# Performance work log

Measured on AMD Instinct MI355X. Metric: run time of the kernel, lower is better.

Reference implementation:

```python
import jax, jax.numpy as jnp
import numpy as np
from jax import lax

N_FRAMES = 256

def _conv(x, w, b):
    # NCHW conv, stride 3 on mel axis (matches MOSNet CNN that collapses mels 81->27->9->3->1)
    y = lax.conv_general_dilated(x, w, window_strides=(1, 3),
                                 padding=((1, 1), (1, 1)),
                                 dimension_numbers=('NCHW', 'OIHW', 'NCHW'))
    return jax.nn.relu(y + b[None, :, None, None])

def _lstm(x, Wih, Whh, bih, bhh, reverse=False):
    # x: [T, B, D] -> hs: [T, B, H]; PyTorch gate order i, f, g, o
    Bsz, H = x.shape[1], Whh.shape[1]
    bias = bih + bhh
    def step(carry, xt):
        h, c = carry
        z = xt @ Wih.T + h @ Whh.T + bias
        i, f, g, o = jnp.split(z, 4, axis=-1)
        c = jax.nn.sigmoid(f) * c + jax.nn.sigmoid(i) * jnp.tanh(g)
        h = jax.nn.sigmoid(o) * jnp.tanh(c)
        return (h, c), h
    init = (jnp.zeros((Bsz, H), x.dtype), jnp.zeros((Bsz, H), x.dtype))
    _, hs = lax.scan(step, init, x, reverse=reverse)
    return hs

def setup_inputs():
    key = jax.random.key(0)
    ks = jax.random.split(key, 24)
    B, T, M = 16, 4096, 81
    chans = [1, 16, 32, 64, 128]
    H = 128
    FC_IN = 2 * H * N_FRAMES  # 65536
    FC_H = 128
    s = 0.05
    inp = {'audio': jax.random.normal(ks[0], (B, T, M), jnp.float32),
           'sample_lengths': jnp.full((B,), T, dtype=jnp.int32)}
    for li in range(4):
        inp['w%d' % li] = jax.random.normal(ks[1 + 2 * li], (chans[li + 1], chans[li], 3, 3), jnp.float32) * s
        inp['b%d' % li] = jnp.zeros((chans[li + 1],), jnp.float32)
    D = chans[-1]
    for d, off in (('f', 9), ('b', 13)):
        inp['Wih_' + d] = jax.random.normal(ks[off], (4 * H, D), jnp.float32) * s
        inp['Whh_' + d] = jax.random.normal(ks[off + 1], (4 * H, H), jnp.float32) * s
        inp['bih_' + d] = jnp.zeros((4 * H,), jnp.float32)
        inp['bhh_' + d] = jnp.zeros((4 * H,), jnp.float32)
    inp['fc1_w'] = jax.random.normal(ks[17], (FC_H, FC_IN), jnp.float32) * 0.005
    inp['fc1_b'] = jnp.zeros((FC_H,), jnp.float32)
    inp['fs_w'] = jax.random.normal(ks[18], (1, FC_H), jnp.float32) * s
    inp['fs_b'] = jnp.zeros((1,), jnp.float32)
    return inp

def reference(audio, w0, b0, w1, b1, w2, b2, w3, b3,
              Wih_f, Whh_f, bih_f, bhh_f, Wih_b, Whh_b, bih_b, bhh_b,
              fc1_w, fc1_b, fs_w, fs_b, sample_lengths):
    B, T, M = audio.shape
    F = T // N_FRAMES  # all lengths == T, multiple of N_FRAMES -> all frames full
    x = audio.reshape(B * F, 1, N_FRAMES, M)   # [BF, 1, nf, mels]
    for w, b in ((w0, b0), (w1, b1), (w2, b2), (w3, b3)):
        x = _conv(x, w, b)                      # mel axis 81->27->9->3->1
    x = x[..., 0].transpose(2, 0, 1)            # [nf, BF, C]
    h_f = _lstm(x, Wih_f, Whh_f, bih_f, bhh_f)
    h_b = _lstm(x, Wih_b, Whh_b, bih_b, bhh_b, reverse=True)
    h = jnp.concatenate([h_f, h_b], axis=-1).transpose(1, 0, 2)  # [BF, nf, 2H]
    flat = h.reshape(B * F, -1)                 # time-major flatten, matches view(1,-1)
    z = jax.nn.relu(flat @ fc1_w.T + fc1_b)     # dropout is identity at inference
    score = jax.nn.sigmoid(z @ fs_w.T + fs_b) * 4.0 + 1.0  # mos range [1,5]
    frames = score.reshape(B, F)
    utt = frames.mean(axis=1)
    return utt, frames
```

## Files before the change

### kernel.cpp

```cpp
#include <hip/hip_runtime.h>
#include <hip/hip_fp16.h>

#define BF 256
#define TSTEPS 256

typedef _Float16 h8_t __attribute__((ext_vector_type(8)));
typedef _Float16 h4_t __attribute__((ext_vector_type(4)));
typedef float f4_t __attribute__((ext_vector_type(4)));

union H8 { uint4 u; h8_t v; };
union H4 { uint2 u; h4_t v; };

static __device__ __forceinline__ float sigmoidf_(float x) {
    return 1.f / (1.f + __expf(-x));
}
static __device__ __forceinline__ float tanhf_(float x) {
    return 1.f - 2.f / (__expf(2.f * x) + 1.f);
}

static __device__ __forceinline__ void pack_one(const float* __restrict__ src,
                                                __half* __restrict__ dst,
                                                int OC, int IC, int KS,
                                                int oc_str, int ic_str, int k_str, int i) {
    int grp = KS / 4;
    int j = i % grp;
    int oc = (i / grp) % OC;
    int g = (i / (grp * OC)) & 3;
    int chunk = i / (grp * OC * 4);
    int CPK = IC / KS;
    int cc = chunk % CPK;
    int khw = chunk / CPK;
    int ic = cc * KS + g * grp + j;
    dst[i] = __float2half(src[(long)oc * oc_str + (long)ic * ic_str + khw * k_str]);
}

__global__ __launch_bounds__(256) void prep_k(
        const float* __restrict__ w0, const float* __restrict__ w1,
        const float* __restrict__ w2, const float* __restrict__ w3,
        const float* __restrict__ Wihf, const float* __restrict__ Wihb,
        const float* __restrict__ Whhf, const float* __restrict__ Whhb,
        float* __restrict__ w0t, __half* __restrict__ w1p,
        __half* __restrict__ w2p, __half* __restrict__ w3p,
        __half* __restrict__ wfp, __half* __restrict__ wbp,
        __half* __restrict__ whhfp, __half* __restrict__ whhbp) {
    int i = blockIdx.x * 256 + threadIdx.x;
    if (i < 144) { int oc = i / 9, rem = i % 9; w0t[rem * 16 + oc] = w0[i]; return; }
    i -= 144;
    if (i < 4608) { pack_one(w1, w1p, 32, 16, 16, 144, 9, 1, i); return; }
    i -= 4608;
    if (i < 18432) { pack_one(w2, w2p, 64, 32, 32, 288, 9, 1, i); return; }
    i -= 18432;
    if (i < 73728) { pack_one(w3, w3p, 128, 64, 32, 576, 9, 1, i); return; }
    i -= 73728;
    if (i < 65536) { pack_one(Wihf, wfp, 512, 128, 32, 128, 1, 0, i); return; }
    i -= 65536;
    if (i < 65536) { pack_one(Wihb, wbp, 512, 128, 32, 128, 1, 0, i); return; }
    i -= 65536;
    if (i < 65536) { pack_one(Whhf, whhfp, 512, 128, 32, 128, 1, 0, i); return; }
    i -= 65536;
    if (i < 65536) { pack_one(Whhb, whhbp, 512, 128, 32, 128, 1, 0, i); return; }
}

__global__ void pack_wf16(const float* __restrict__ src, __half* __restrict__ dst,
                          int OC, int IC, int KS,
                          int oc_str, int ic_str, int k_str, int total) {
    int i = blockIdx.x * 256 + threadIdx.x;
    if (i >= total) return;
    pack_one(src, dst, OC, IC, KS, oc_str, ic_str, k_str, i);
}

__global__ __launch_bounds__(256) void conv0_k(const float* __restrict__ in,
                                               const float* __restrict__ wT,
                                               const float* __restrict__ bias,
                                               __half* __restrict__ out) {
    __shared__ float wsm[9][16];
    __shared__ float bs[16];
    int tid = threadIdx.x;
    if (tid < 144) wsm[tid / 16][tid % 16] = wT[tid];
    if (tid < 16) bs[tid] = bias[tid];
    __syncthreads();
    int gid = blockIdx.x * 256 + tid;
    int ow = gid % 27;
    int t = (gid / 27) % 256;
    int bf = gid / (27 * 256);
    float acc[16];
#pragma unroll
    for (int o = 0; o < 16; o++) acc[o] = bs[o];
    int iw0 = ow * 3 - 1;
#pragma unroll
    for (int kh = 0; kh < 3; kh++) {
        int tt = t + kh - 1;
        if ((unsigned)tt >= 256u) continue;
        const float* ip = in + ((long)bf * 256 + tt) * 81;
#pragma unroll
        for (int kw = 0; kw < 3; kw++) {
            int iw = iw0 + kw;
            if ((unsigned)iw >= 81u) continue;
            float x = ip[iw];
#pragma unroll
            for (int o = 0; o < 16; o++) acc[o] += x * wsm[kh * 3 + kw][o];
        }
    }
    __half2* op = (__half2*)(out + (long)gid * 16);
#pragma unroll
    for (int o = 0; o < 8; o++)
        op[o] = __floats2half2_rn(fmaxf(acc[2 * o], 0.f), fmaxf(acc[2 * o + 1], 0.f));
}

template<int IC, int OC, int WIN, int WOUT, int KS>
__global__ __launch_bounds__(256) void convM_k(const __half* __restrict__ in,
                                               const __half* __restrict__ wp,
                                               const float* __restrict__ bias,
                                               __half* __restrict__ out) {
    constexpr int NT = OC / 16;
    constexpr int CPK = IC / KS;
    constexpr int NCHUNK = 9 * CPK;
    constexpr int GRP = KS / 4;
    int tid = threadIdx.x;
    int lane = tid & 63;
    int wv = tid >> 6;
    int l15 = lane & 15;
    int g = lane >> 4;
    int m = blockIdx.x * 64 + wv * 16 + l15;
    int ow = m % WOUT;
    int t = (m / WOUT) % 256;
    int bf = m / (WOUT * 256);

    f4_t acc[NT];
#pragma unroll
    for (int nt = 0; nt < NT; nt++)
#pragma unroll
        for (int r = 0; r < 4; r++) acc[nt][r] = 0.f;

#pragma unroll
    for (int chunk = 0; chunk < NCHUNK; chunk++) {
        int khw = chunk / CPK, cc = chunk % CPK;
        int kh = khw / 3;
        int kw = khw - kh * 3;
        int tt = t + kh - 1;
        int iw = ow * 3 + kw - 1;
        bool ok = ((unsigned)tt < 256u) && ((unsigned)iw < (unsigned)WIN);
        long aoff = ok ? (((long)(bf * 256 + tt) * WIN + iw) * IC + cc * KS + g * GRP) : 0;
        if constexpr (KS == 32) {
            H8 af;
            af.u = *(const uint4*)(in + aoff);
            if (!ok) af.u = make_uint4(0u, 0u, 0u, 0u);
#pragma unroll
            for (int nt = 0; nt < NT; nt++) {
                H8 bf8;
                bf8.u = *(const uint4*)(wp + ((long)(chunk * 4 + g) * OC + nt * 16 + l15) * GRP);
                acc[nt] = __builtin_amdgcn_mfma_f32_16x16x32_f16(af.v, bf8.v, acc[nt], 0, 0, 0);
            }
        } else {
            H4 af;
            af.u = *(const uint2*)(in + aoff);
            if (!ok) af.u = make_uint2(0u, 0u);
#pragma unroll
            for (int nt = 0; nt < NT; nt++) {
                H4 bf4;
                bf4.u = *(const uint2*)(wp + ((long)(chunk * 4 + g) * OC + nt * 16 + l15) * GRP);
                acc[nt] = __builtin_amdgcn_mfma_f32_16x16x16f16(af.v, bf4.v, acc[nt], 0, 0, 0);
            }
        }
    }
    int orow = blockIdx.x * 64 + wv * 16 + g * 4;
#pragma unroll
    for (int nt = 0; nt < NT; nt++) {
        int oc = nt * 16 + l15;
        float b = bias[oc];
#pragma unroll
        for (int r = 0; r < 4; r++) {
            float v = fmaxf(acc[nt][r] + b, 0.f);
            out[(long)(orow + r) * OC + oc] = __float2half(v);
        }
    }
}

__global__ __launch_bounds__(256) void gates_k(const __half* __restrict__ X,
                                               const __half* __restrict__ wpf,
                                               const __half* __restrict__ wpb,
                                               const float* __restrict__ bf1,
                                               const float* __restrict__ bf2,
                                               const float* __restrict__ bb1,
                                               const float* __restrict__ bb2,
                                               __half* __restrict__ Gf,
                                               __half* __restrict__ Gb) {
    int dir = blockIdx.z;
    const __half* wp = dir ? wpb : wpf;
    const float* b1 = dir ? bb1 : bf1;
    const float* b2 = dir ? bb2 : bf2;
    __half* G = dir ? Gb : Gf;
    int tid = threadIdx.x;
    int lane = tid & 63;
    int wv = tid >> 6;
    int l15 = lane & 15;
    int g = lane >> 4;
    long r0 = (long)blockIdx.x * 128 + wv * 32;
    int n0 = blockIdx.y * 128;

    f4_t acc[2][8];
#pragma unroll
    for (int s = 0; s < 2; s++)
#pragma unroll
        for (int nt = 0; nt < 8; nt++)
#pragma unroll
            for (int r = 0; r < 4; r++) acc[s][nt][r] = 0.f;

#pragma unroll
    for (int chunk = 0; chunk < 4; chunk++) {
        H8 a0, a1;
        a0.u = *(const uint4*)(X + (r0 + l15) * 128 + chunk * 32 + g * 8);
        a1.u = *(const uint4*)(X + (r0 + 16 + l15) * 128 + chunk * 32 + g * 8);
#pragma unroll
        for (int nt = 0; nt < 8; nt++) {
            H8 bw;
            bw.u = *(const uint4*)(wp + ((long)(chunk * 4 + g) * 512 + n0 + nt * 16 + l15) * 8);
            acc[0][nt] = __builtin_amdgcn_mfma_f32_16x16x32_f16(a0.v, bw.v, acc[0][nt], 0, 0, 0);
            acc[1][nt] = __builtin_amdgcn_mfma_f32_16x16x32_f16(a1.v, bw.v, acc[1][nt], 0, 0, 0);
        }
    }
#pragma unroll
    for (int nt = 0; nt < 8; nt++) {
        int col = n0 + nt * 16 + l15;
        float bias = b1[col] + b2[col];
#pragma unroll
        for (int s = 0; s < 2; s++) {
            long row = r0 + s * 16 + g * 4;
#pragma unroll
            for (int r = 0; r < 4; r++)
                G[(row + r) * 512 + col] = __float2half(acc[s][nt][r] + bias);
        }
    }
}

__global__ __launch_bounds__(512, 2) void lstm_k(const __half* __restrict__ Gf,
                                                 const __half* __restrict__ Gb,
                                                 const __half* __restrict__ whhfp,
                                                 const __half* __restrict__ whhbp,
                                                 __half* __restrict__ flat) {
    int bid = blockIdx.x;
    int dir = bid >> 7;
    int b0 = (bid & 127) * 2;
    const __half* G = dir ? Gb : Gf;
    const __half* wp = dir ? whhbp : whhfp;
    int tid = threadIdx.x;
    int w = tid >> 6;
    int lane = tid & 63;
    int l15 = lane & 15;
    int g2 = lane >> 4;
    int chn = l15 >> 3;
    int r = l15 & 3;
    bool wr = (l15 & 4) == 0;
    int ua = w * 16 + g2 * 4 + r;

    H8 afr[4][4];
#pragma unroll
    for (int k = 0; k < 4; k++) {
        int gate = k * 128 + w * 16 + l15;
#pragma unroll
        for (int c = 0; c < 4; c++)
            afr[k][c].u = *(const uint4*)(wp + ((long)((c * 4 + g2) * 512 + gate)) * 8);
    }

    __shared__ __half hbuf[2][2][128];
    if (tid < 256) hbuf[0][tid >> 7][tid & 127] = __float2half(0.f);
    __syncthreads();

    long grow = (long)(b0 + chn) * 256;
    int stepd = dir ? -1 : 1;
    int ts = dir ? 255 : 0;
    __half gcur[4], gnxt[4];
#pragma unroll
    for (int k = 0; k < 4; k++)
        gcur[k] = G[(grow + ts) * 512 + k * 128 + ua];
    float cstate = 0.f;

    for (int t = 0; t < 256; t++) {
        int tsn = (t == 255) ? ts : (ts + stepd);
#pragma unroll
        for (int k = 0; k < 4; k++)
            gnxt[k] = G[(grow + tsn) * 512 + k * 128 + ua];

        int p = t & 1;
        H8 bfr[4];
#pragma unroll
        for (int c = 0; c < 4; c++)
            bfr[c].u = *(const uint4*)(&hbuf[p][chn][c * 32 + g2 * 8]);

        f4_t acc[4];
#pragma unroll
        for (int k = 0; k < 4; k++)
#pragma unroll
            for (int rr = 0; rr < 4; rr++) acc[k][rr] = 0.f;
#pragma unroll
        for (int c = 0; c < 4; c++)
#pragma unroll
            for (int k = 0; k < 4; k++)
                acc[k] = __builtin_amdgcn_mfma_f32_16x16x32_f16(afr[k][c].v, bfr[c].v,
                                                                acc[k], 0, 0, 0);
        float z[4];
#pragma unroll
        for (int k = 0; k < 4; k++) {
            f4_t a = acc[k];
            float lo = (r & 1) ? a[1] : a[0];
            float hi = (r & 1) ? a[3] : a[2];
            z[k] = ((r & 2) ? hi : lo) + __half2float(gcur[k]);
        }
        float ig = sigmoidf_(z[0]), fg = sigmoidf_(z[1]);
        float gg = tanhf_(z[2]), og = sigmoidf_(z[3]);
        cstate = fg * cstate + ig * gg;
        float h = og * tanhf_(cstate);
        __half hh = __float2half(h);
        if (wr) {
            hbuf[p ^ 1][chn][ua] = hh;
            flat[(long)(b0 + chn) * 65536 + ts * 256 + dir * 128 + ua] = hh;
        }
        __syncthreads();
#pragma unroll
        for (int k = 0; k < 4; k++) gcur[k] = gnxt[k];
        ts = tsn;
    }
}

__global__ __launch_bounds__(256) void fc1m_k(const __half* __restrict__ flat,
                                              const __half* __restrict__ wp,
                                              float* __restrict__ z) {
    int tid = threadIdx.x;
    int lane = tid & 63;
    int wv = tid >> 6;
    int l15 = lane & 15;
    int g = lane >> 4;
    int m0 = blockIdx.x * 64 + wv * 16;
    long k0 = (long)blockIdx.y * 1024;

    f4_t acc[8];
#pragma unroll
    for (int nt = 0; nt < 8; nt++)
#pragma unroll
        for (int r = 0; r < 4; r++) acc[nt][r] = 0.f;

    for (int c = 0; c < 32; c++) {
        long chunk = (k0 >> 5) + c;
        H8 af;
        af.u = *(const uint4*)(flat + (long)(m0 + l15) * 65536 + k0 + c * 32 + g * 8);
#pragma unroll
        for (int nt = 0; nt < 8; nt++) {
            H8 bw;
            bw.u = *(const uint4*)(wp + ((chunk * 4 + g) * 128 + nt * 16 + l15) * 8);
            acc[nt] = __builtin_amdgcn_mfma_f32_16x16x32_f16(af.v, bw.v, acc[nt], 0, 0, 0);
        }
    }
#pragma unroll
    for (int nt = 0; nt < 8; nt++)
#pragma unroll
        for (int r = 0; r < 4; r++)
            atomicAdd(&z[(m0 + g * 4 + r) * 128 + nt * 16 + l15], acc[nt][r]);
}

__global__ void zero_k(float* __restrict__ p, int n) {
    int i = blockIdx.x * 256 + threadIdx.x;
    if (i < n) p[i] = 0.f;
}

__global__ __launch_bounds__(256) void head_k(const float* __restrict__ z,
                                              const float* __restrict__ b1,
                                              const float* __restrict__ fsw,
                                              const float* __restrict__ fsb,
                                              float* __restrict__ out) {
    __shared__ float sf[256];
    int r = threadIdx.x;
    float acc = fsb[0];
#pragma unroll
    for (int j4 = 0; j4 < 32; j4++) {
        float4 zv = *(const float4*)&z[r * 128 + j4 * 4];
        float4 bv = *(const float4*)&b1[j4 * 4];
        float4 wv = *(const float4*)&fsw[j4 * 4];
        acc += fmaxf(zv.x + bv.x, 0.f) * wv.x;
        acc += fmaxf(zv.y + bv.y, 0.f) * wv.y;
        acc += fmaxf(zv.z + bv.z, 0.f) * wv.z;
        acc += fmaxf(zv.w + bv.w, 0.f) * wv.w;
    }
    float val = sigmoidf_(acc) * 4.f + 1.f;
    out[16 + r] = val;
    sf[r] = val;
    __syncthreads();
    if (r < 16) {
        float m = 0.f;
#pragma unroll
        for (int f = 0; f < 16; f++) m += sf[r * 16 + f];
        out[r] = m * (1.f / 16.f);
    }
}

extern "C" void kernel_launch(void* const* d_in, const int* in_sizes, int n_in,
                              void* d_out, int out_size, void* d_ws, size_t ws_size,
                              hipStream_t stream) {
    const float* audio = (const float*)d_in[0];
    const float* w0 = (const float*)d_in[2];
    const float* b0 = (const float*)d_in[3];
    const float* w1 = (const float*)d_in[4];
    const float* b1 = (const float*)d_in[5];
    const float* w2 = (const float*)d_in[6];
    const float* b2 = (const float*)d_in[7];
    const float* w3 = (const float*)d_in[8];
    const float* b3 = (const float*)d_in[9];
    const float* Wih_f = (const float*)d_in[10];
    const float* Whh_f = (const float*)d_in[11];
    const float* bih_f = (const float*)d_in[12];
    const float* bhh_f = (const float*)d_in[13];
    const float* Wih_b = (const float*)d_in[14];
    const float* Whh_b = (const float*)d_in[15];
    const float* bih_b = (const float*)d_in[16];
    const float* bhh_b = (const float*)d_in[17];
    const float* fc1_w = (const float*)d_in[18];
    const float* fc1_b = (const float*)d_in[19];
    const float* fs_w = (const float*)d_in[20];
    const float* fs_b = (const float*)d_in[21];
    float* out = (float*)d_out;

    char* ws = (char*)d_ws;
    __half* Gf    = (__half*)(ws);
    __half* out1  = (__half*)(ws);
    __half* fc1p  = (__half*)(ws);
    __half* Gb    = (__half*)(ws + 67108864);
    __half* flat16= (__half*)(ws + 134217728);
    __half* out0  = (__half*)(ws + 134217728);
    __half* X     = (__half*)(ws + 201326592);
    __half* out2  = (__half*)(ws + 218103808);
    char* rd = ws + 243269632;
    float*  w0t   = (float*)(rd);
    __half* w1p   = (__half*)(rd + 1024);
    __half* w2p   = (__half*)(rd + 10240);
    __half* w3p   = (__half*)(rd + 47104);
    __half* wfp   = (__half*)(rd + 194560);
    __half* wbp   = (__half*)(rd + 325632);
    __half* whhfp = (__half*)(rd + 456704);
    __half* whhbp = (__half*)(rd + 587776);
    float*  zbuf  = (float*)(rd + 718848);

    prep_k<<<1403, 256, 0, stream>>>(w0, w1, w2, w3, Wih_f, Wih_b, Whh_f, Whh_b,
                                     w0t, w1p, w2p, w3p, wfp, wbp, whhfp, whhbp);

    conv0_k<<<6912, 256, 0, stream>>>(audio, w0t, b0, out0);
    convM_k<16, 32, 27, 9, 16><<<9216, 256, 0, stream>>>(out0, w1p, b1, out1);
    convM_k<32, 64, 9, 3, 32><<<3072, 256, 0, stream>>>(out1, w2p, b2, out2);
    convM_k<64, 128, 3, 1, 32><<<1024, 256, 0, stream>>>(out2, w3p, b3, X);

    gates_k<<<dim3(512, 4, 2), 256, 0, stream>>>(X, wfp, wbp, bih_f, bhh_f,
                                                 bih_b, bhh_b, Gf, Gb);

    lstm_k<<<256, 512, 0, stream>>>(Gf, Gb, whhfp, whhbp, flat16);

    pack_wf16<<<32768, 256, 0, stream>>>(fc1_w, fc1p, 128, 65536, 32, 65536, 1, 0, 8388608);
    zero_k<<<128, 256, 0, stream>>>(zbuf, 256 * 128);
    fc1m_k<<<dim3(4, 64), 256, 0, stream>>>(flat16, fc1p, zbuf);
    head_k<<<1, 256, 0, stream>>>(zbuf, fc1_b, fs_w, fs_b, out);
}
```

Baseline: 559.5 us.

## Transpose gate buffer to time-contiguous layout and split LSTM gate math across lanes

```diff
diff --git a/kernel.cpp b/kernel.cpp
--- a/kernel.cpp
+++ b/kernel.cpp
@@ -10,6 +10,7 @@
 
 union H8 { uint4 u; h8_t v; };
 union H4 { uint2 u; h4_t v; };
+union U2H4 { uint2 u; __half h[4]; };
 
 static __device__ __forceinline__ float sigmoidf_(float x) {
     return 1.f / (1.f + __expf(-x));
@@ -219,16 +220,25 @@
             acc[1][nt] = __builtin_amdgcn_mfma_f32_16x16x32_f16(a1.v, bw.v, acc[1][nt], 0, 0, 0);
         }
     }
+    int b = (int)(r0 >> 8);
 #pragma unroll
     for (int nt = 0; nt < 8; nt++) {
         int col = n0 + nt * 16 + l15;
         float bias = b1[col] + b2[col];
+        long base = ((long)b * 512 + col) * 256;
 #pragma unroll
         for (int s = 0; s < 2; s++) {
-            long row = r0 + s * 16 + g * 4;
-#pragma unroll
-            for (int r = 0; r < 4; r++)
-                G[(row + r) * 512 + col] = __float2half(acc[s][nt][r] + bias);
+            int tb = (int)(r0 & 255) + s * 16 + g * 4;
+            U2H4 pk;
+            if (!dir) {
+#pragma unroll
+                for (int r = 0; r < 4; r++) pk.h[r] = __float2half(acc[s][nt][r] + bias);
+                *(uint2*)(G + base + tb) = pk.u;
+            } else {
+#pragma unroll
+                for (int r = 0; r < 4; r++) pk.h[3 - r] = __float2half(acc[s][nt][r] + bias);
+                *(uint2*)(G + base + (252 - tb)) = pk.u;
+            }
         }
     }
 }
@@ -250,8 +260,9 @@
     int g2 = lane >> 4;
     int chn = l15 >> 3;
     int r = l15 & 3;
-    bool wr = (l15 & 4) == 0;
+    int bit2 = (l15 >> 2) & 1;
     int ua = w * 16 + g2 * 4 + r;
+    bool wrt = bit2 && ((r & 1) == 0);
 
     H8 afr[4][4];
 #pragma unroll
@@ -262,63 +273,84 @@
             afr[k][c].u = *(const uint4*)(wp + ((long)((c * 4 + g2) * 512 + gate)) * 8);
     }
 
-    __shared__ __half hbuf[2][2][128];
+    __shared__ __align__(16) __half hbuf[2][2][128];
     if (tid < 256) hbuf[0][tid >> 7][tid & 127] = __float2half(0.f);
     __syncthreads();
 
-    long grow = (long)(b0 + chn) * 256;
-    int stepd = dir ? -1 : 1;
-    int ts = dir ? 255 : 0;
-    __half gcur[4], gnxt[4];
-#pragma unroll
-    for (int k = 0; k < 4; k++)
-        gcur[k] = G[(grow + ts) * 512 + k * 128 + ua];
-    float cstate = 0.f;
-
-    for (int t = 0; t < 256; t++) {
-        int tsn = (t == 255) ? ts : (ts + stepd);
-#pragma unroll
-        for (int k = 0; k < 4; k++)
-            gnxt[k] = G[(grow + tsn) * 512 + k * 128 + ua];
-
-        int p = t & 1;
-        H8 bfr[4];
-#pragma unroll
-        for (int c = 0; c < 4; c++)
-            bfr[c].u = *(const uint4*)(&hbuf[p][chn][c * 32 + g2 * 8]);
-
-        f4_t acc[4];
-#pragma unroll
-        for (int k = 0; k < 4; k++)
-#pragma unroll
-            for (int rr = 0; rr < 4; rr++) acc[k][rr] = 0.f;
-#pragma unroll
-        for (int c = 0; c < 4; c++)
+    const __half* gb0 = G + (((long)(b0 + chn) * 512) + bit2 * 256 + ua) * 256;
+    const __half* gb1 = gb0 + 128 * 256;
+
+    float cst = 0.f;
+    float ma = bit2 ? 2.f : 1.f;
+    float mb = bit2 ? 2.f : 1.f;
+    float cb = bit2 ? -1.f : 0.f;
+    const f4_t zero4 = {0.f, 0.f, 0.f, 0.f};
+
+    H8 gc0, gc1, gn0, gn1;
+    gc0.u = *(const uint4*)(gb0);
+    gc1.u = *(const uint4*)(gb1);
+    long fbase = (long)(b0 + chn) * 65536 + dir * 128 + ua;
+
+    for (int to = 0; to < 32; to++) {
+        if (to < 31) {
+            gn0.u = *(const uint4*)(gb0 + (to + 1) * 8);
+            gn1.u = *(const uint4*)(gb1 + (to + 1) * 8);
+        }
+#pragma unroll
+        for (int ti = 0; ti < 8; ti++) {
+            int s = to * 8 + ti;
+            int p = s & 1;
+            H8 bfr[4];
+#pragma unroll
+            for (int c = 0; c < 4; c++)
+                bfr[c].u = *(const uint4*)(&hbuf[p][chn][c * 32 + g2 * 8]);
+
+            f4_t acc[4];
 #pragma unroll
             for (int k = 0; k < 4; k++)
-                acc[k] = __builtin_amdgcn_mfma_f32_16x16x32_f16(afr[k][c].v, bfr[c].v,
-                                                                acc[k], 0, 0, 0);
-        float z[4];
-#pragma unroll
-        for (int k = 0; k < 4; k++) {
-            f4_t a = acc[k];
-            float lo = (r & 1) ? a[1] : a[0];
-            float hi = (r & 1) ? a[3] : a[2];
-            z[k] = ((r & 2) ? hi : lo) + __half2float(gcur[k]);
-        }
-        float ig = sigmoidf_(z[0]), fg = sigmoidf_(z[1]);
-        float gg = tanhf_(z[2]), og = sigmoidf_(z[3]);
-        cstate = fg * cstate + ig * gg;
-        float h = og * tanhf_(cstate);
-        __half hh = __float2half(h);
-        if (wr) {
-            hbuf[p ^ 1][chn][ua] = hh;
-            flat[(long)(b0 + chn) * 65536 + ts * 256 + dir * 128 + ua] = hh;
-        }
-        __syncthreads();
-#pragma unroll
-        for (int k = 0; k < 4; k++) gcur[k] = gnxt[k];
-        ts = tsn;
+                acc[k] = __builtin_amdgcn_mfma_f32_16x16x32_f16(afr[k][0].v, bfr[0].v,
+                                                                zero4, 0, 0, 0);
+#pragma unroll
+            for (int c = 1; c < 4; c++)
+#pragma unroll
+                for (int k = 0; k < 4; k++)
+                    acc[k] = __builtin_amdgcn_mfma_f32_16x16x32_f16(afr[k][c].v, bfr[c].v,
+                                                                    acc[k], 0, 0, 0);
+            f4_t aA, aB;
+#pragma unroll
+            for (int e = 0; e < 4; e++) {
+                aA[e] = bit2 ? acc[2][e] : acc[0][e];
+                aB[e] = bit2 ? acc[3][e] : acc[1][e];
+            }
+            float loA = (r & 1) ? aA[1] : aA[0];
+            float hiA = (r & 1) ? aA[3] : aA[2];
+            float eA = (r & 2) ? hiA : loA;
+            float loB = (r & 1) ? aB[1] : aB[0];
+            float hiB = (r & 1) ? aB[3] : aB[2];
+            float eB = (r & 2) ? hiB : loB;
+
+            float za = eA + (float)gc0.v[ti];
+            float zb = eB + (float)gc1.v[ti];
+            float sa = sigmoidf_(ma * za);
+            float fa = sa * mb + cb;
+            float sb = sigmoidf_(zb);
+            float grecv = __shfl_xor(fa, 4, 64);
+            float cn = sb * cst + fa * grecv;
+            cst = cn;
+            float tc = tanhf_(cn);
+            float tcr = __shfl_xor(tc, 4, 64);
+            float h = sb * tcr;
+            float hp = __shfl_xor(h, 1, 64);
+            if (wrt) {
+                __half2 h2 = __floats2half2_rn(h, hp);
+                int ts = dir ? (255 - s) : s;
+                *(__half2*)(&hbuf[p ^ 1][chn][ua]) = h2;
+                *(__half2*)(flat + fbase + (long)ts * 256) = h2;
+            }
+            __syncthreads();
+        }
+        gc0 = gn0;
+        gc1 = gn1;
     }
 }
 
```

New measurement: 535.5 us. 1.04x faster.
